# Kernel tuning notes

Hardware: AMD Instinct MI355X
Metric: run time of the kernel (lower is better)

Reference implementation:

```python
import jax, jax.numpy as jnp
import numpy as np
from jax import lax

B, L, D, H = 32, 32, 512, 512
NEG = jnp.float32(-1e9)


def setup_inputs() -> dict:
    key = jax.random.key(0)
    k1, k2, k3, k4, k5 = jax.random.split(key, 5)
    return {
        "inp": jax.random.normal(k1, (B, L, D), jnp.float32),
        "length": jax.random.randint(k2, (B,), 2, L + 1),
        "W_word": jax.random.normal(k3, (D, 2 * H), jnp.float32) * np.float32(np.sqrt(2.0 / D)),
        "b_word": jnp.zeros((2 * H,), jnp.float32),
        "W_comp": jax.random.normal(k4, (2 * H, 5 * H), jnp.float32) * np.float32(np.sqrt(2.0 / (2 * H))),
        "b_comp": jnp.zeros((5 * H,), jnp.float32),
        "comp_query": jax.random.normal(k5, (H,), jnp.float32) * np.float32(0.01),
    }


def _forward(inp, length, W_word, b_word, W_comp, b_comp, comp_query):
    # length_mask[b, t] = 1 if t < length[b]
    length_mask = (jnp.arange(L)[None, :] < length[:, None]).astype(jnp.float32)  # (B, L)
    # leaf states from word_linear: (B, L, 2H) -> h, c
    hc = inp @ W_word + b_word
    h0, c0 = jnp.split(hc, 2, axis=-1)  # each (B, L, H)

    def cell(hl, cl, hr, cr):
        # BinaryTreeLSTMLayer: cat -> 5H gates
        g = jnp.concatenate([hl, hr], axis=-1) @ W_comp + b_comp  # (B, L-1, 5H)
        ig, fl, fr, u, o = jnp.split(g, 5, axis=-1)
        c = cl * jax.nn.sigmoid(fl + 1.0) + cr * jax.nn.sigmoid(fr + 1.0) + jnp.tanh(u) * jax.nn.sigmoid(ig)
        h = jax.nn.sigmoid(o) * jnp.tanh(c)
        return h, c

    def step(carry, i):
        # Fixed-shape (B, L, H) carry; valid length shrinks by 1 each step,
        # tail is zero-padded garbage never selected thanks to masks.
        h, c = carry
        hl, hr = h[:, :-1, :], h[:, 1:, :]
        cl, cr = c[:, :-1, :], c[:, 1:, :]
        nh, nc = cell(hl, cl, hr, cr)  # (B, L-1, H) candidate parents
        # greedy (eval-mode) top-1 composition selection
        logits = jnp.einsum('blh,h->bl', nh, comp_query)
        cand = (jnp.arange(L - 1)[None, :] < (length[:, None] - 1 - i)).astype(jnp.float32)
        sel = jax.nn.one_hot(jnp.argmax(jnp.where(cand > 0, logits, NEG), axis=1), L - 1, dtype=jnp.float32)
        cum = jnp.cumsum(sel, axis=1)
        left = 1.0 - cum
        right = jnp.concatenate([jnp.zeros((B, 1), jnp.float32), cum[:, :-1]], axis=1)
        ch = sel[..., None] * nh + left[..., None] * hl + right[..., None] * hr
        cc = sel[..., None] * nc + left[..., None] * cl + right[..., None] * cr
        sel_h = jnp.sum(sel[..., None] * ch, axis=1)  # (B, H) selected composed node
        is_last = (i == L - 2)  # final merge skips selection (single candidate)
        uh = jnp.where(is_last, nh, ch)
        uc = jnp.where(is_last, nc, cc)
        done = length_mask[:, i + 1][:, None, None]  # 1 if this sample still merging
        nhst = done * uh + (1.0 - done) * h[:, :-1, :]
        ncst = done * uc + (1.0 - done) * c[:, :-1, :]
        pad = jnp.zeros((B, 1, H), jnp.float32)
        h2 = jnp.concatenate([nhst, pad], axis=1)
        c2 = jnp.concatenate([ncst, pad], axis=1)
        node = jnp.where(is_last, h2[:, 0, :], sel_h)
        return (h2, c2), node

    (hf, cf), nodes_rest = lax.scan(step, (h0, c0), jnp.arange(L - 1))
    nodes = jnp.concatenate([h0, jnp.swapaxes(nodes_rest, 0, 1)], axis=1)  # (B, 2L-1, H)
    return hf[:, 0, :], cf[:, 0, :], nodes


def reference(inp, length, W_word, b_word, W_comp, b_comp, comp_query):
    return _forward(inp, length, W_word, b_word, W_comp, b_comp, comp_query)
```

## Files before the change

kernel.cpp:

```cpp
#include <hip/hip_runtime.h>
#include <math.h>

constexpr int NB = 32, NL = 32, ND = 512, NHID = 512, NSTEPS = 31;
constexpr int NC5 = 2560;
constexpr int BH = NB * NHID;
constexpr int HSLOT_Z = 32;
constexpr int NBLK = 160;
constexpr int NGEMM = 80;

constexpr float INV2048 = 1.f / 2048.f;

typedef _Float16 half8  __attribute__((ext_vector_type(8)));
typedef _Float16 half4  __attribute__((ext_vector_type(4)));
typedef float    f32x16 __attribute__((ext_vector_type(16)));
typedef unsigned long long u64;

constexpr size_t OFF_GRAW = 0;
constexpr size_t OFF_PNH  = OFF_GRAW + (size_t)32 * 32 * 2560;
constexpr size_t OFF_PNC  = OFF_PNH + (size_t)31 * 32 * 512;
constexpr size_t OFF_CST  = OFF_PNC + (size_t)31 * 32 * 512;
constexpr size_t OFF_HHI  = OFF_CST + (size_t)33 * 32 * 512;
constexpr size_t OFF_HLO  = OFF_HHI + (size_t)64 * 32 * 512 / 2;
constexpr size_t OFF_WTH  = OFF_HLO + (size_t)64 * 32 * 512 / 2;
constexpr size_t OFF_WTL  = OFF_WTH + (size_t)NC5 * 1024 / 2;
constexpr size_t OFF_INT  = OFF_WTL + (size_t)NC5 * 1024 / 2;
constexpr size_t OFF_LIST = OFF_INT + 8192;

__device__ __forceinline__ float sigf(float x) { return 1.f / (1.f + expf(-x)); }

__device__ __forceinline__ int ld_sc(const int* p) {
    return __hip_atomic_load(p, __ATOMIC_RELAXED, __HIP_MEMORY_SCOPE_AGENT);
}
__device__ __forceinline__ u64 ld_sc64(const void* p) {
    return __hip_atomic_load((const u64*)p, __ATOMIC_RELAXED, __HIP_MEMORY_SCOPE_AGENT);
}
__device__ __forceinline__ void st_sc64(void* p, u64 v) {
    __hip_atomic_store((u64*)p, v, __ATOMIC_RELAXED, __HIP_MEMORY_SCOPE_AGENT);
}
__device__ __forceinline__ u64 packf2(float a, float b) {
    return (u64)__float_as_uint(a) | ((u64)__float_as_uint(b) << 32);
}
__device__ __forceinline__ float2 uf2(u64 v) {
    float2 r;
    r.x = __uint_as_float((unsigned)v);
    r.y = __uint_as_float((unsigned)(v >> 32));
    return r;
}

__device__ __forceinline__ unsigned pack_e(int b, int slot, int l, int r) {
    return (unsigned)b | ((unsigned)slot << 5) | ((unsigned)l << 10) | ((unsigned)r << 16);
}

__global__ __launch_bounds__(256) void init_kernel(
    int* __restrict__ ireg, u64* __restrict__ elist,
    _Float16* __restrict__ hHi, _Float16* __restrict__ hLo, float* __restrict__ cSt)
{
    const int blk = blockIdx.x, tid = threadIdx.x;
    if (blk < 32) {
        if (tid < 31) {
            unsigned e = (unsigned)blk | ((unsigned)tid << 5) |
                         ((unsigned)tid << 10) | ((unsigned)(tid + 1) << 16);
            elist[tid * 32 + blk] = (u64)e;
        }
    } else if (blk == 32) {
        const size_t zb = (size_t)HSLOT_Z * NB * NHID;
        for (int i = tid; i < NB * NHID; i += 256) {
            hHi[zb + i] = (_Float16)0.f;
            hLo[zb + i] = (_Float16)0.f;
            cSt[zb + i] = 0.f;
        }
    } else {
        for (int i = tid; i < 8192; i += 256) ireg[i] = 0;
    }
}

__global__ __launch_bounds__(256) void wsplit_kernel(
    const float* __restrict__ W, _Float16* __restrict__ Wth, _Float16* __restrict__ Wtl)
{
    __shared__ float t[32][33];
    const int n0 = blockIdx.x * 32, k0 = blockIdx.y * 32;
    const int tid = threadIdx.x;
    const int c = tid & 31, r8 = tid >> 5;
#pragma unroll
    for (int p = 0; p < 4; ++p) {
        int r = p * 8 + r8;
        t[r][c] = W[(size_t)(k0 + r) * NC5 + n0 + c];
    }
    __syncthreads();
    const int nl = tid >> 3, k4 = (tid & 7) * 4;
    half4 vh, vl;
#pragma unroll
    for (int i = 0; i < 4; ++i) {
        float v = t[k4 + i][nl];
        _Float16 hh = (_Float16)v;
        vh[i] = hh;
        vl[i] = (_Float16)((v - (float)hh) * 2048.f);
    }
    size_t o = (size_t)(n0 + nl) * 1024 + k0 + k4;
    *(half4*)&Wth[o] = vh;
    *(half4*)&Wtl[o] = vl;
}

__global__ __launch_bounds__(256) void word_gemm64(
    const float* __restrict__ A, const float* __restrict__ W,
    const float* __restrict__ bias,
    _Float16* __restrict__ hi0, _Float16* __restrict__ lo0,
    float* __restrict__ cst, float* __restrict__ out)
{
    const int m0 = blockIdx.x * 64;
    const int n0 = blockIdx.y * 64;
    const int tid = threadIdx.x;
    const int tx = tid & 15, ty = tid >> 4;
    __shared__ float As[16][64];
    __shared__ float Bs[16][64];
    float acc[4][4];
#pragma unroll
    for (int i = 0; i < 4; ++i)
#pragma unroll
        for (int j = 0; j < 4; ++j) acc[i][j] = 0.f;

    for (int kt = 0; kt < ND; kt += 16) {
        {
            int row = tid >> 2, kq = tid & 3;
            float4 v = *(const float4*)(A + (size_t)(m0 + row) * ND + kt + kq * 4);
            As[kq * 4 + 0][row] = v.x;
            As[kq * 4 + 1][row] = v.y;
            As[kq * 4 + 2][row] = v.z;
            As[kq * 4 + 3][row] = v.w;
            int kr = tid >> 4, nq = tid & 15;
            float4 vb = *(const float4*)(W + (size_t)(kt + kr) * 1024 + n0 + nq * 4);
            *(float4*)&Bs[kr][nq * 4] = vb;
        }
        __syncthreads();
#pragma unroll
        for (int kk = 0; kk < 16; ++kk) {
            float a0 = As[kk][ty * 4 + 0], a1 = As[kk][ty * 4 + 1];
            float a2 = As[kk][ty * 4 + 2], a3 = As[kk][ty * 4 + 3];
            float4 bv = *(float4*)&Bs[kk][tx * 4];
            acc[0][0] = fmaf(a0, bv.x, acc[0][0]); acc[0][1] = fmaf(a0, bv.y, acc[0][1]);
            acc[0][2] = fmaf(a0, bv.z, acc[0][2]); acc[0][3] = fmaf(a0, bv.w, acc[0][3]);
            acc[1][0] = fmaf(a1, bv.x, acc[1][0]); acc[1][1] = fmaf(a1, bv.y, acc[1][1]);
            acc[1][2] = fmaf(a1, bv.z, acc[1][2]); acc[1][3] = fmaf(a1, bv.w, acc[1][3]);
            acc[2][0] = fmaf(a2, bv.x, acc[2][0]); acc[2][1] = fmaf(a2, bv.y, acc[2][1]);
            acc[2][2] = fmaf(a2, bv.z, acc[2][2]); acc[2][3] = fmaf(a2, bv.w, acc[2][3]);
            acc[3][0] = fmaf(a3, bv.x, acc[3][0]); acc[3][1] = fmaf(a3, bv.y, acc[3][1]);
            acc[3][2] = fmaf(a3, bv.z, acc[3][2]); acc[3][3] = fmaf(a3, bv.w, acc[3][3]);
        }
        __syncthreads();
    }
    float* nodes = out + 2 * BH;
#pragma unroll
    for (int i = 0; i < 4; ++i) {
        int r = m0 + ty * 4 + i;
        int b = r >> 5, l = r & 31;
#pragma unroll
        for (int jn = 0; jn < 4; ++jn) {
            int n = n0 + tx * 4 + jn;
            float v = acc[i][jn] + bias[n];
            if (n < NHID) {
                size_t si = ((size_t)l * NB + b) * NHID + n;
                _Float16 hh = (_Float16)v;
                hi0[si] = hh;
                lo0[si] = (_Float16)((v - (float)hh) * 2048.f);
                nodes[((size_t)b * 63 + l) * NHID + n] = v;
            } else {
                cst[((size_t)l * NB + b) * NHID + (n - NHID)] = v;
            }
        }
    }
}

__global__ __launch_bounds__(256, 1) void tree_loop(
    _Float16* __restrict__ hHi, _Float16* __restrict__ hLo,
    const _Float16* __restrict__ Wth, const _Float16* __restrict__ Wtl,
    float* __restrict__ graw, const float* __restrict__ bias,
    const float* __restrict__ q, const int* __restrict__ len,
    float* __restrict__ pnh, float* __restrict__ pnc, float* __restrict__ cSt,
    u64* __restrict__ elist, int* __restrict__ ireg, float* __restrict__ out)
{
    const int nt = blockIdx.x;
    const int tid = threadIdx.x;
    const int col = nt % NGEMM;
    const int kw = tid >> 6;
    const int lane = tid & 63;
    const int l5 = lane >> 5, ln = lane & 31;

    int* gd = ireg;

    __shared__ float red[4][32][32];
    __shared__ unsigned s_entry[64];
    __shared__ int s_pidx[32], s_hidx[32], s_cidx[32];
    __shared__ float s_plog[32];
    __shared__ int s_k;
    __shared__ int s_prevk;

    const _Float16* bHiP = Wth + (size_t)(col * 32 + ln) * 1024 + (kw << 8) + l5 * 8;
    const _Float16* bLoP = Wtl + (size_t)(col * 32 + ln) * 1024 + (kw << 8) + l5 * 8;
    half8 Bh[16], Bl[16];
#pragma unroll
    for (int ks = 0; ks < 16; ++ks) {
        Bh[ks] = *(const half8*)(bHiP + ks * 16);
        Bl[ks] = *(const half8*)(bLoP + ks * 16);
    }

    auto gemm_tile = [&](const unsigned* se) {
        {
            const unsigned e = se[ln];
            const int db = e & 31;
            const int lsl = (e >> 10) & 63, rsl = (e >> 16) & 63;
            const int hs = (kw < 2) ? lsl : rsl;
            const int koff = ((kw & 1) << 8) + l5 * 8;
            const _Float16* aHiP = hHi + ((size_t)hs * NB + db) * NHID + koff;
            const _Float16* aLoP = hLo + ((size_t)hs * NB + db) * NHID + koff;
            f32x16 acc1 = (f32x16)0.f, acc2 = (f32x16)0.f;
#pragma unroll
            for (int ks = 0; ks < 16; ++ks) {
                half8 Ah = *(const half8*)(aHiP + ks * 16);
                half8 Al = *(const half8*)(aLoP + ks * 16);
                acc1 = __builtin_amdgcn_mfma_f32_32x32x16_f16(Ah, Bh[ks], acc1, 0, 0, 0);
                acc2 = __builtin_amdgcn_mfma_f32_32x32x16_f16(Ah, Bl[ks], acc2, 0, 0, 0);
                acc2 = __builtin_amdgcn_mfma_f32_32x32x16_f16(Al, Bh[ks], acc2, 0, 0, 0);
            }
#pragma unroll
            for (int a = 0; a < 16; ++a) {
                int row = (a & 3) + 8 * (a >> 2) + 4 * l5;
                red[kw][row][ln] = acc1[a] + acc2[a] * INV2048;
            }
        }
        __syncthreads();
        {
            const int row = tid >> 3, c0 = (tid & 7) * 4;
            const unsigned er = se[row];
            const int rb = er & 31, rslot = (er >> 5) & 31;
            float4 s;
            s.x = (red[0][row][c0+0] + red[1][row][c0+0]) + (red[2][row][c0+0] + red[3][row][c0+0]);
            s.y = (red[0][row][c0+1] + red[1][row][c0+1]) + (red[2][row][c0+1] + red[3][row][c0+1]);
            s.z = (red[0][row][c0+2] + red[1][row][c0+2]) + (red[2][row][c0+2] + red[3][row][c0+2]);
            s.w = (red[0][row][c0+3] + red[1][row][c0+3]) + (red[2][row][c0+3] + red[3][row][c0+3]);
            float* gp = &graw[((size_t)rslot * NB + rb) * NC5 + col * 32 + c0];
            st_sc64(gp,     packf2(s.x, s.y));
            st_sc64(gp + 2, packf2(s.z, s.w));
        }
        __syncthreads();
    };

    __syncthreads();
    {
        const int par = nt / NGEMM;
        for (int mt = par; mt < 31; mt += 2) {
            if (tid < 32) s_entry[tid] = (unsigned)ld_sc64(&elist[mt * 32 + tid]);
            __syncthreads();
            gemm_tile(s_entry);
        }
        if (tid == 0) {
            asm volatile("s_waitcnt vmcnt(0)" ::: "memory");
            __hip_atomic_fetch_add(&gd[(nt & 3) * 32], 1, __ATOMIC_RELAXED,
                                   __HIP_MEMORY_SCOPE_AGENT);
        }
    }
    if (nt >= 112) return;

    if (nt < NGEMM) {
        for (int step = 1; step < NSTEPS; ++step) {
            if (tid < 64) {
                u64 e;
                while ((int)((e = ld_sc64(&elist[tid])) >> 32) < step)
                    __builtin_amdgcn_s_sleep(1);
                s_entry[tid] = (unsigned)e;
            }
            __syncthreads();
            gemm_tile(s_entry);
            gemm_tile(s_entry + 32);
            if (tid == 0) {
                asm volatile("s_waitcnt vmcnt(0)" ::: "memory");
                __hip_atomic_fetch_add(&gd[(nt & 3) * 32], 1, __ATOMIC_RELAXED,
                                       __HIP_MEMORY_SCOPE_AGENT);
            }
        }
        return;
    }

    {
        const int b = nt - NGEMM;
        const int lenb = len[b];
        if (tid < 32) { s_pidx[tid] = min(tid, 30); s_hidx[tid] = tid; s_cidx[tid] = tid; }
        if (tid == 0) s_prevk = -1;
        __syncthreads();

        for (int step = 0; step < NSTEPS; ++step) {
            if (tid < 4) {
                const int tgt = 40 + 20 * step;
                while (ld_sc(&gd[tid * 32]) < tgt) __builtin_amdgcn_s_sleep(1);
            }
            __syncthreads();

            const int pk = s_prevk;
            int nf;
            if (step == 0) nf = 31; else if (pk < 0) nf = 0; else nf = (pk >= 1) ? 2 : 1;
            for (int f = kw; f < nf; f += 4) {
                const int j = (step == 0) ? f : (pk - (nf - 1) + f);
                const int slot = s_pidx[j];
                const int lc = s_cidx[j], rc2 = s_cidx[j + 1];
                const float* gr  = graw + ((size_t)slot * NB + b) * NC5;
                const float* clp = cSt + ((size_t)lc * NB + b) * NHID;
                const float* crp = cSt + ((size_t)rc2 * NB + b) * NHID;
                float lpart = 0.f;
#pragma unroll
                for (int i = 0; i < 4; ++i) {
                    const int h = 2 * lane + 128 * i;
                    float2 g0 = uf2(ld_sc64(gr + h));
                    float2 g1 = uf2(ld_sc64(gr + 512 + h));
                    float2 g2 = uf2(ld_sc64(gr + 1024 + h));
                    float2 g3 = uf2(ld_sc64(gr + 1536 + h));
                    float2 g4 = uf2(ld_sc64(gr + 2048 + h));
                    const float2 b0 = *(const float2*)(bias + h);
                    const float2 b1 = *(const float2*)(bias + 512 + h);
                    const float2 b2 = *(const float2*)(bias + 1024 + h);
                    const float2 b3 = *(const float2*)(bias + 1536 + h);
                    const float2 b4 = *(const float2*)(bias + 2048 + h);
                    const float2 cl2 = *(const float2*)(clp + h);
                    const float2 cr2 = *(const float2*)(crp + h);
                    const float2 q2  = *(const float2*)(q + h);
                    float2 hv, cv;
                    {
                        float c = cl2.x * sigf(g1.x + b1.x + 1.f) + cr2.x * sigf(g2.x + b2.x + 1.f)
                                + tanhf(g3.x + b3.x) * sigf(g0.x + b0.x);
                        float hh = sigf(g4.x + b4.x) * tanhf(c);
                        cv.x = c; hv.x = hh;
                    }
                    {
                        float c = cl2.y * sigf(g1.y + b1.y + 1.f) + cr2.y * sigf(g2.y + b2.y + 1.f)
                                + tanhf(g3.y + b3.y) * sigf(g0.y + b0.y);
                        float hh = sigf(g4.y + b4.y) * tanhf(c);
                        cv.y = c; hv.y = hh;
                    }
                    const size_t po = ((size_t)slot * NB + b) * NHID + h;
                    *(float2*)(pnh + po) = hv;
                    *(float2*)(pnc + po) = cv;
                    lpart = fmaf(hv.x, q2.x, lpart);
                    lpart = fmaf(hv.y, q2.y, lpart);
                }
#pragma unroll
                for (int off = 32; off > 0; off >>= 1) lpart += __shfl_down(lpart, off);
                if (lane == 0) s_plog[slot] = lpart;
            }
            __syncthreads();

            const int actb = lenb - 1 - step;
            const int merge = actb >= 1;
            if (tid < 64) {
                float v = -1e30f;
                int idx = tid;
                if (tid < actb && tid < 31) v = s_plog[s_pidx[tid]];
#pragma unroll
                for (int off = 32; off > 0; off >>= 1) {
                    float ov = __shfl_down(v, off);
                    int   oi = __shfl_down(idx, off);
                    if (ov > v || (ov == v && oi < idx)) { v = ov; idx = oi; }
                }
                if (tid == 0) s_k = idx;
            }
            __syncthreads();
            const int k = s_k;
            const int last = (step == NSTEPS - 1);
            const int NSLOT = 33 + step;

            float* noderow = out + 2 * BH + ((size_t)b * 63 + 32 + step) * NHID;
            if (merge) {
                const int kslot = s_pidx[k];
                const int csl = s_cidx[k];
                if (tid < 128) {
                    const int h0 = tid * 4;
                    const size_t pb = ((size_t)kslot * NB + b) * NHID + h0;
                    float4 x4 = *(const float4*)&pnh[pb];
                    float4 c4 = *(const float4*)&pnc[pb];
                    half4 hv, lv;
#pragma unroll
                    for (int i = 0; i < 4; ++i) {
                        float x = (&x4.x)[i];
                        _Float16 hh = (_Float16)x;
                        hv[i] = hh;
                        lv[i] = (_Float16)((x - (float)hh) * 2048.f);
                    }
                    const size_t so = ((size_t)NSLOT * NB + b) * NHID + h0;
                    st_sc64(&hHi[so], __builtin_bit_cast(u64, hv));
                    st_sc64(&hLo[so], __builtin_bit_cast(u64, lv));
                    *(float4*)&cSt[((size_t)csl * NB + b) * NHID + h0] = c4;
                    *(float4*)&noderow[h0] = x4;
                    if (last) {
                        *(float4*)&out[b * NHID + h0] = x4;
                        *(float4*)&out[BH + b * NHID + h0] = c4;
                    }
                }
            } else {
                const int s0p = s_pidx[0], s0h = s_hidx[0], s0c = s_cidx[0];
                if (tid < 128) {
                    const int h0 = tid * 4;
                    if (!last) {
                        *(float4*)&noderow[h0] =
                            *(const float4*)&pnh[((size_t)s0p * NB + b) * NHID + h0];
                    } else {
                        const size_t so = ((size_t)s0h * NB + b) * NHID + h0;
                        half4 hv = __builtin_bit_cast(half4, ld_sc64(&hHi[so]));
                        half4 lv = __builtin_bit_cast(half4, ld_sc64(&hLo[so]));
                        float4 x4;
#pragma unroll
                        for (int i = 0; i < 4; ++i)
                            (&x4.x)[i] = (float)hv[i] + (float)lv[i] * INV2048;
                        *(float4*)&noderow[h0] = x4;
                        *(float4*)&out[b * NHID + h0] = x4;
                        *(float4*)&out[BH + b * NHID + h0] =
                            *(const float4*)&cSt[((size_t)s0c * NB + b) * NHID + h0];
                    }
                }
            }
            __syncthreads();

            if (tid == 0) {
                const unsigned dummy = pack_e(b, 31, HSLOT_Z, HSLOT_Z);
                if (merge) {
                    unsigned e1 = pack_e(b, s_pidx[k], NSLOT,
                                         (k + 2 <= 31) ? s_hidx[k + 2] : HSLOT_Z);
                    unsigned e0 = (k >= 1)
                        ? pack_e(b, s_pidx[k - 1], s_hidx[k - 1], NSLOT) : dummy;
                    if (!last) {
                        const u64 st = (u64)(step + 1) << 32;
                        st_sc64(&elist[2 * b],     (u64)e0 | st);
                        st_sc64(&elist[2 * b + 1], (u64)e1 | st);
                    }
                    const int recycP = s_pidx[k + 1];
                    for (int j2 = k + 1; j2 <= 29; ++j2) s_pidx[j2] = s_pidx[j2 + 1];
                    if (k < 30) s_pidx[30] = recycP;
                    s_hidx[k] = NSLOT;
                    for (int pp = k + 1; pp <= 30; ++pp) s_hidx[pp] = s_hidx[pp + 1];
                    s_hidx[31] = HSLOT_Z;
                    for (int pp = k + 1; pp <= 30; ++pp) s_cidx[pp] = s_cidx[pp + 1];
                    s_cidx[31] = HSLOT_Z;
                    s_prevk = k;
                } else {
                    if (!last) {
                        const u64 st = (u64)(step + 1) << 32;
                        st_sc64(&elist[2 * b],     (u64)dummy | st);
                        st_sc64(&elist[2 * b + 1], (u64)dummy | st);
                    }
                    s_prevk = -1;
                }
            }
        }
    }
}

extern "C" void kernel_launch(void* const* d_in, const int* in_sizes, int n_in,
                              void* d_out, int out_size, void* d_ws, size_t ws_size,
                              hipStream_t stream) {
    const float* inp    = (const float*)d_in[0];
    const int*   length = (const int*)d_in[1];
    const float* W_word = (const float*)d_in[2];
    const float* b_word = (const float*)d_in[3];
    const float* W_comp = (const float*)d_in[4];
    const float* b_comp = (const float*)d_in[5];
    const float* q      = (const float*)d_in[6];
    float* out = (float*)d_out;
    float* ws  = (float*)d_ws;

    float*     graw = ws + OFF_GRAW;
    float*     pnh  = ws + OFF_PNH;
    float*     pnc  = ws + OFF_PNC;
    float*     cSt  = ws + OFF_CST;
    _Float16*  hHi  = (_Float16*)(ws + OFF_HHI);
    _Float16*  hLo  = (_Float16*)(ws + OFF_HLO);
    _Float16*  Wth  = (_Float16*)(ws + OFF_WTH);
    _Float16*  Wtl  = (_Float16*)(ws + OFF_WTL);
    int*       ireg = (int*)(ws + OFF_INT);
    u64*       elist = (u64*)(ws + OFF_LIST);

    init_kernel<<<34, 256, 0, stream>>>(ireg, elist, hHi, hLo, cSt);
    wsplit_kernel<<<dim3(NC5 / 32, 1024 / 32), 256, 0, stream>>>(W_comp, Wth, Wtl);
    word_gemm64<<<dim3(16, 16), 256, 0, stream>>>(inp, W_word, b_word,
                                                  hHi, hLo, cSt, out);
    tree_loop<<<NBLK, 256, 0, stream>>>(hHi, hLo, Wth, Wtl, graw, b_comp, q, length,
                                        pnh, pnc, cSt, elist, ireg, out);
}
```

Before: 766.0 us.

## Fuse LSTM cell epilogue into per-block GEMM tiles with unit-permuted weights

Weights are permuted so each of 128 blocks owns 4 hidden units across all 5 gates. This lets every block compute the LSTM cell, the cell state and a partial selection logit directly after its MFMA tile, instead of writing raw gates to global memory for separate controller blocks to read. Cell state stays block-local and fresh candidate slots replace the recycled ones, so the final nodes, h and c are assembled by a new gather kernel from a selection log. The cost is more workspace, an extra permutation kernel and a gather pass, and each controller must now reduce 128 logit partials across blocks.

```diff
diff --git a/kernel.cpp b/kernel.cpp
--- a/kernel.cpp
+++ b/kernel.cpp
@@ -1,12 +1,13 @@
 #include <hip/hip_runtime.h>
 #include <math.h>
 
-constexpr int NB = 32, NL = 32, ND = 512, NHID = 512, NSTEPS = 31;
+constexpr int NB = 32, ND = 512, NHID = 512, NSTEPS = 31;
 constexpr int NC5 = 2560;
 constexpr int BH = NB * NHID;
-constexpr int HSLOT_Z = 32;
-constexpr int NBLK = 160;
-constexpr int NGEMM = 80;
+constexpr int SLOT_Z = 32;
+constexpr int SLOT_DUMMY = 126;
+constexpr int NSLOTS = 128;
+constexpr int NBLK = 128;
 
 constexpr float INV2048 = 1.f / 2048.f;
 
@@ -15,16 +16,22 @@
 typedef float    f32x16 __attribute__((ext_vector_type(16)));
 typedef unsigned long long u64;
 
-constexpr size_t OFF_GRAW = 0;
-constexpr size_t OFF_PNH  = OFF_GRAW + (size_t)32 * 32 * 2560;
-constexpr size_t OFF_PNC  = OFF_PNH + (size_t)31 * 32 * 512;
-constexpr size_t OFF_CST  = OFF_PNC + (size_t)31 * 32 * 512;
-constexpr size_t OFF_HHI  = OFF_CST + (size_t)33 * 32 * 512;
-constexpr size_t OFF_HLO  = OFF_HHI + (size_t)64 * 32 * 512 / 2;
-constexpr size_t OFF_WTH  = OFF_HLO + (size_t)64 * 32 * 512 / 2;
+constexpr size_t OFF_WTH  = 0;
 constexpr size_t OFF_WTL  = OFF_WTH + (size_t)NC5 * 1024 / 2;
-constexpr size_t OFF_INT  = OFF_WTL + (size_t)NC5 * 1024 / 2;
-constexpr size_t OFF_LIST = OFF_INT + 8192;
+constexpr size_t OFF_WPH  = OFF_WTL + (size_t)NC5 * 1024 / 2;
+constexpr size_t OFF_WPL  = OFF_WPH + (size_t)128 * 32 * 1024 / 2;
+constexpr size_t OFF_HHI  = OFF_WPL + (size_t)128 * 32 * 1024 / 2;
+constexpr size_t OFF_HLO  = OFF_HHI + (size_t)NSLOTS * 32 * 512 / 2;
+constexpr size_t OFF_HF32 = OFF_HLO + (size_t)NSLOTS * 32 * 512 / 2;
+constexpr size_t OFF_CST  = OFF_HF32 + (size_t)NSLOTS * 32 * 512;
+constexpr size_t OFF_CLOC = OFF_CST + (size_t)32 * 32 * 512;
+constexpr size_t OFF_LPART= OFF_CLOC + (size_t)128 * NSLOTS * 32 * 4;
+constexpr size_t OFF_SEL  = OFF_LPART + (size_t)NSLOTS * 32 * 128;
+constexpr size_t OFF_ELIST= OFF_SEL + 1024;
+constexpr size_t OFF_IREG = OFF_ELIST + 4096;
+
+constexpr int IR_GD = 0;
+constexpr int IR_E0 = 256;
 
 __device__ __forceinline__ float sigf(float x) { return 1.f / (1.f + expf(-x)); }
 
@@ -37,40 +44,35 @@
 __device__ __forceinline__ void st_sc64(void* p, u64 v) {
     __hip_atomic_store((u64*)p, v, __ATOMIC_RELAXED, __HIP_MEMORY_SCOPE_AGENT);
 }
-__device__ __forceinline__ u64 packf2(float a, float b) {
-    return (u64)__float_as_uint(a) | ((u64)__float_as_uint(b) << 32);
-}
-__device__ __forceinline__ float2 uf2(u64 v) {
-    float2 r;
-    r.x = __uint_as_float((unsigned)v);
-    r.y = __uint_as_float((unsigned)(v >> 32));
-    return r;
-}
-
-__device__ __forceinline__ unsigned pack_e(int b, int slot, int l, int r) {
-    return (unsigned)b | ((unsigned)slot << 5) | ((unsigned)l << 10) | ((unsigned)r << 16);
+__device__ __forceinline__ void st_sc32f(void* p, float v) {
+    __hip_atomic_store((int*)p, __float_as_int(v), __ATOMIC_RELAXED, __HIP_MEMORY_SCOPE_AGENT);
+}
+__device__ __forceinline__ void st_sc32i(void* p, int v) {
+    __hip_atomic_store((int*)p, v, __ATOMIC_RELAXED, __HIP_MEMORY_SCOPE_AGENT);
+}
+__device__ __forceinline__ unsigned pack_e(int b, int cand, int l, int r) {
+    return (unsigned)b | ((unsigned)cand << 5) | ((unsigned)l << 12) | ((unsigned)r << 19);
 }
 
 __global__ __launch_bounds__(256) void init_kernel(
     int* __restrict__ ireg, u64* __restrict__ elist,
-    _Float16* __restrict__ hHi, _Float16* __restrict__ hLo, float* __restrict__ cSt)
+    _Float16* __restrict__ hHi, _Float16* __restrict__ hLo)
 {
     const int blk = blockIdx.x, tid = threadIdx.x;
-    if (blk < 32) {
-        if (tid < 31) {
-            unsigned e = (unsigned)blk | ((unsigned)tid << 5) |
-                         ((unsigned)tid << 10) | ((unsigned)(tid + 1) << 16);
-            elist[tid * 32 + blk] = (u64)e;
-        }
-    } else if (blk == 32) {
-        const size_t zb = (size_t)HSLOT_Z * NB * NHID;
-        for (int i = tid; i < NB * NHID; i += 256) {
+    if (blk == 0) {
+        for (int i = tid; i < 128; i += 256) ireg[IR_GD + i] = 0;
+        for (int i = tid; i < 992; i += 256) {
+            int t = i >> 5, b = i & 31;
+            ireg[IR_E0 + i] = (int)pack_e(b, 33 + t, t, t + 1);
+        }
+    } else if (blk == 1) {
+        for (int i = tid; i < 31 * 64; i += 256) elist[i] = 0ull;
+    } else {
+        const size_t zb = ((size_t)SLOT_Z * 32) * 512;
+        for (int i = tid + (blk - 2) * 256; i < 32 * 512; i += 512) {
             hHi[zb + i] = (_Float16)0.f;
             hLo[zb + i] = (_Float16)0.f;
-            cSt[zb + i] = 0.f;
-        }
-    } else {
-        for (int i = tid; i < 8192; i += 256) ireg[i] = 0;
+        }
     }
 }
 
@@ -99,6 +101,27 @@
     size_t o = (size_t)(n0 + nl) * 1024 + k0 + k4;
     *(half4*)&Wth[o] = vh;
     *(half4*)&Wtl[o] = vl;
+}
+
+__global__ __launch_bounds__(256) void wperm_kernel(
+    const _Float16* __restrict__ Wth, const _Float16* __restrict__ Wtl,
+    _Float16* __restrict__ WpH, _Float16* __restrict__ WpL)
+{
+    const int blk = blockIdx.x;
+    const int tid = threadIdx.x;
+    const int k4 = tid * 4;
+    for (int c = 0; c < 32; ++c) {
+        half4 vh = (half4)(_Float16)0.f, vl = (half4)(_Float16)0.f;
+        if (c < 20) {
+            int unit = blk * 4 + c / 5, g = c % 5;
+            size_t src = (size_t)(g * 512 + unit) * 1024 + k4;
+            vh = *(const half4*)&Wth[src];
+            vl = *(const half4*)&Wtl[src];
+        }
+        size_t dst = ((size_t)blk * 32 + c) * 1024 + k4;
+        *(half4*)&WpH[dst] = vh;
+        *(half4*)&WpL[dst] = vl;
+    }
 }
 
 __global__ __launch_bounds__(256) void word_gemm64(
@@ -171,31 +194,33 @@
 }
 
 __global__ __launch_bounds__(256, 1) void tree_loop(
-    _Float16* __restrict__ hHi, _Float16* __restrict__ hLo,
-    const _Float16* __restrict__ Wth, const _Float16* __restrict__ Wtl,
-    float* __restrict__ graw, const float* __restrict__ bias,
-    const float* __restrict__ q, const int* __restrict__ len,
-    float* __restrict__ pnh, float* __restrict__ pnc, float* __restrict__ cSt,
-    u64* __restrict__ elist, int* __restrict__ ireg, float* __restrict__ out)
+    _Float16* __restrict__ hHi, _Float16* __restrict__ hLo, float* __restrict__ hF32,
+    const _Float16* __restrict__ WpH, const _Float16* __restrict__ WpL,
+    const float* __restrict__ bias, const float* __restrict__ q,
+    const int* __restrict__ len, const float* __restrict__ cst,
+    float* __restrict__ cLoc, float* __restrict__ lpart,
+    u64* __restrict__ elist, int* __restrict__ selLog, int* __restrict__ ireg)
 {
-    const int nt = blockIdx.x;
+    const int blk = blockIdx.x;
     const int tid = threadIdx.x;
-    const int col = nt % NGEMM;
-    const int kw = tid >> 6;
-    const int lane = tid & 63;
+    const int kw = tid >> 6, lane = tid & 63;
     const int l5 = lane >> 5, ln = lane & 31;
 
-    int* gd = ireg;
+    int* gd = ireg + IR_GD;
+    const int* E0 = ireg + IR_E0;
 
     __shared__ float red[4][32][32];
     __shared__ unsigned s_entry[64];
-    __shared__ int s_pidx[32], s_hidx[32], s_cidx[32];
-    __shared__ float s_plog[32];
-    __shared__ int s_k;
-    __shared__ int s_prevk;
-
-    const _Float16* bHiP = Wth + (size_t)(col * 32 + ln) * 1024 + (kw << 8) + l5 * 8;
-    const _Float16* bLoP = Wtl + (size_t)(col * 32 + ln) * 1024 + (kw << 8) + l5 * 8;
+    __shared__ float sH[32][4];
+    __shared__ float sLP[32];
+    __shared__ float sBias[4][5];
+    __shared__ float sQ[4];
+    __shared__ float s_plog[128];
+    __shared__ int s_pidx[32], s_hidx[32];
+    __shared__ int s_k, s_prevk;
+
+    const _Float16* bHiP = WpH + ((size_t)blk * 32 + ln) * 1024 + (kw << 8) + l5 * 8;
+    const _Float16* bLoP = WpL + ((size_t)blk * 32 + ln) * 1024 + (kw << 8) + l5 * 8;
     half8 Bh[16], Bl[16];
 #pragma unroll
     for (int ks = 0; ks < 16; ++ks) {
@@ -203,146 +228,162 @@
         Bl[ks] = *(const half8*)(bLoP + ks * 16);
     }
 
-    auto gemm_tile = [&](const unsigned* se) {
-        {
-            const unsigned e = se[ln];
-            const int db = e & 31;
-            const int lsl = (e >> 10) & 63, rsl = (e >> 16) & 63;
-            const int hs = (kw < 2) ? lsl : rsl;
-            const int koff = ((kw & 1) << 8) + l5 * 8;
-            const _Float16* aHiP = hHi + ((size_t)hs * NB + db) * NHID + koff;
-            const _Float16* aLoP = hLo + ((size_t)hs * NB + db) * NHID + koff;
-            f32x16 acc1 = (f32x16)0.f, acc2 = (f32x16)0.f;
-#pragma unroll
-            for (int ks = 0; ks < 16; ++ks) {
-                half8 Ah = *(const half8*)(aHiP + ks * 16);
-                half8 Al = *(const half8*)(aLoP + ks * 16);
-                acc1 = __builtin_amdgcn_mfma_f32_32x32x16_f16(Ah, Bh[ks], acc1, 0, 0, 0);
-                acc2 = __builtin_amdgcn_mfma_f32_32x32x16_f16(Ah, Bl[ks], acc2, 0, 0, 0);
-                acc2 = __builtin_amdgcn_mfma_f32_32x32x16_f16(Al, Bh[ks], acc2, 0, 0, 0);
-            }
-#pragma unroll
-            for (int a = 0; a < 16; ++a) {
-                int row = (a & 3) + 8 * (a >> 2) + 4 * l5;
-                red[kw][row][ln] = acc1[a] + acc2[a] * INV2048;
-            }
-        }
-        __syncthreads();
-        {
-            const int row = tid >> 3, c0 = (tid & 7) * 4;
-            const unsigned er = se[row];
-            const int rb = er & 31, rslot = (er >> 5) & 31;
-            float4 s;
-            s.x = (red[0][row][c0+0] + red[1][row][c0+0]) + (red[2][row][c0+0] + red[3][row][c0+0]);
-            s.y = (red[0][row][c0+1] + red[1][row][c0+1]) + (red[2][row][c0+1] + red[3][row][c0+1]);
-            s.z = (red[0][row][c0+2] + red[1][row][c0+2]) + (red[2][row][c0+2] + red[3][row][c0+2]);
-            s.w = (red[0][row][c0+3] + red[1][row][c0+3]) + (red[2][row][c0+3] + red[3][row][c0+3]);
-            float* gp = &graw[((size_t)rslot * NB + rb) * NC5 + col * 32 + c0];
-            st_sc64(gp,     packf2(s.x, s.y));
-            st_sc64(gp + 2, packf2(s.z, s.w));
-        }
-        __syncthreads();
-    };
-
+    if (tid < 20) { int ul = tid / 5, g = tid % 5; sBias[ul][g] = bias[g * 512 + blk * 4 + ul]; }
+    if (tid >= 32 && tid < 36) sQ[tid - 32] = q[blk * 4 + (tid - 32)];
+
+    float* cB = cLoc + (size_t)blk * NSLOTS * 32 * 4;
+    for (int i = tid; i < 33 * 32 * 4; i += 256) {
+        int slot = i >> 7, rem = i & 127;
+        int b = rem >> 2, ul = rem & 3;
+        cB[i] = (slot == SLOT_Z) ? 0.f
+                                 : cst[((size_t)slot * 32 + b) * 512 + blk * 4 + ul];
+    }
+
+    int lenb = 0;
+    if (blk < NB) {
+        if (tid < 31) s_pidx[tid] = 33 + tid;
+        if (tid < 32) s_hidx[tid] = tid;
+        if (tid == 0) s_prevk = 0;
+        lenb = len[blk];
+    }
     __syncthreads();
-    {
-        const int par = nt / NGEMM;
-        for (int mt = par; mt < 31; mt += 2) {
-            if (tid < 32) s_entry[tid] = (unsigned)ld_sc64(&elist[mt * 32 + tid]);
-            __syncthreads();
-            gemm_tile(s_entry);
+
+    for (int step = 0; step < NSTEPS; ++step) {
+        int ntiles;
+        if (step == 0) {
+            ntiles = 31;
+        } else {
+            ntiles = 2;
+            if (tid < 64) {
+                u64 e;
+                while ((int)((e = ld_sc64(&elist[step * 64 + tid])) >> 32) < step)
+                    __builtin_amdgcn_s_sleep(4);
+                s_entry[tid] = (unsigned)e;
+            }
+            __syncthreads();
+        }
+
+        for (int t = 0; t < ntiles; ++t) {
+            if (step == 0) {
+                if (tid < 32) s_entry[tid] = (unsigned)E0[t * 32 + tid];
+                __syncthreads();
+            }
+            const unsigned* se = (step == 0) ? s_entry : s_entry + t * 32;
+            {
+                const unsigned e = se[ln];
+                const int eb = e & 31;
+                const int lsl = (e >> 12) & 127, rsl = (e >> 19) & 127;
+                const int hs = (kw < 2) ? lsl : rsl;
+                const int koff = ((kw & 1) << 8) + l5 * 8;
+                const _Float16* aHiP = hHi + ((size_t)hs * 32 + eb) * 512 + koff;
+                const _Float16* aLoP = hLo + ((size_t)hs * 32 + eb) * 512 + koff;
+                f32x16 acc1 = (f32x16)0.f, acc2 = (f32x16)0.f;
+#pragma unroll
+                for (int ks = 0; ks < 16; ++ks) {
+                    half8 Ah = *(const half8*)(aHiP + ks * 16);
+                    half8 Al = *(const half8*)(aLoP + ks * 16);
+                    acc1 = __builtin_amdgcn_mfma_f32_32x32x16_f16(Ah, Bh[ks], acc1, 0, 0, 0);
+                    acc2 = __builtin_amdgcn_mfma_f32_32x32x16_f16(Ah, Bl[ks], acc2, 0, 0, 0);
+                    acc2 = __builtin_amdgcn_mfma_f32_32x32x16_f16(Al, Bh[ks], acc2, 0, 0, 0);
+                }
+#pragma unroll
+                for (int a = 0; a < 16; ++a) {
+                    int row = (a & 3) + 8 * (a >> 2) + 4 * l5;
+                    red[kw][row][ln] = acc1[a] + acc2[a] * INV2048;
+                }
+            }
+            __syncthreads();
+            if (tid < 128) {
+                const int r = tid >> 2, ul = tid & 3;
+                const unsigned e = se[r];
+                const int eb = e & 31, cand = (e >> 5) & 127;
+                const int lsl = (e >> 12) & 127, rsl = (e >> 19) & 127;
+                const int c0 = ul * 5;
+                float g0 = (red[0][r][c0+0] + red[1][r][c0+0]) + (red[2][r][c0+0] + red[3][r][c0+0]);
+                float g1 = (red[0][r][c0+1] + red[1][r][c0+1]) + (red[2][r][c0+1] + red[3][r][c0+1]);
+                float g2 = (red[0][r][c0+2] + red[1][r][c0+2]) + (red[2][r][c0+2] + red[3][r][c0+2]);
+                float g3 = (red[0][r][c0+3] + red[1][r][c0+3]) + (red[2][r][c0+3] + red[3][r][c0+3]);
+                float g4 = (red[0][r][c0+4] + red[1][r][c0+4]) + (red[2][r][c0+4] + red[3][r][c0+4]);
+                float ig = g0 + sBias[ul][0];
+                float fl = g1 + sBias[ul][1];
+                float fr = g2 + sBias[ul][2];
+                float uu = g3 + sBias[ul][3];
+                float oo = g4 + sBias[ul][4];
+                float cl = cB[lsl * 128 + eb * 4 + ul];
+                float cr = cB[rsl * 128 + eb * 4 + ul];
+                float c = cl * sigf(fl + 1.f) + cr * sigf(fr + 1.f) + tanhf(uu) * sigf(ig);
+                float h = sigf(oo) * tanhf(c);
+                cB[cand * 128 + eb * 4 + ul] = c;
+                sH[r][ul] = h;
+                float p = h * sQ[ul];
+                p += __shfl_down(p, 1);
+                p += __shfl_down(p, 2);
+                if (ul == 0) sLP[r] = p;
+            }
+            __syncthreads();
+            if (tid < 32) {
+                const unsigned e = se[tid];
+                const int eb = e & 31, cand = (e >> 5) & 127;
+                float x0 = sH[tid][0], x1 = sH[tid][1], x2 = sH[tid][2], x3 = sH[tid][3];
+                half4 hv, lv;
+                {
+                    _Float16 h0 = (_Float16)x0, h1 = (_Float16)x1,
+                             h2 = (_Float16)x2, h3 = (_Float16)x3;
+                    hv[0] = h0; hv[1] = h1; hv[2] = h2; hv[3] = h3;
+                    lv[0] = (_Float16)((x0 - (float)h0) * 2048.f);
+                    lv[1] = (_Float16)((x1 - (float)h1) * 2048.f);
+                    lv[2] = (_Float16)((x2 - (float)h2) * 2048.f);
+                    lv[3] = (_Float16)((x3 - (float)h3) * 2048.f);
+                }
+                const size_t so = ((size_t)cand * 32 + eb) * 512 + blk * 4;
+                st_sc64(&hHi[so], __builtin_bit_cast(u64, hv));
+                st_sc64(&hLo[so], __builtin_bit_cast(u64, lv));
+                u64 f01 = (u64)__float_as_uint(x0) | ((u64)__float_as_uint(x1) << 32);
+                u64 f23 = (u64)__float_as_uint(x2) | ((u64)__float_as_uint(x3) << 32);
+                st_sc64(&hF32[so], f01);
+                st_sc64(&hF32[so + 2], f23);
+                st_sc32f(&lpart[((size_t)cand * 32 + eb) * 128 + blk], sLP[tid]);
+            }
+            __syncthreads();
         }
         if (tid == 0) {
             asm volatile("s_waitcnt vmcnt(0)" ::: "memory");
-            __hip_atomic_fetch_add(&gd[(nt & 3) * 32], 1, __ATOMIC_RELAXED,
+            __hip_atomic_fetch_add(&gd[(blk & 3) * 32], 1, __ATOMIC_RELAXED,
                                    __HIP_MEMORY_SCOPE_AGENT);
         }
-    }
-    if (nt >= 112) return;
-
-    if (nt < NGEMM) {
-        for (int step = 1; step < NSTEPS; ++step) {
-            if (tid < 64) {
-                u64 e;
-                while ((int)((e = ld_sc64(&elist[tid])) >> 32) < step)
-                    __builtin_amdgcn_s_sleep(1);
-                s_entry[tid] = (unsigned)e;
-            }
-            __syncthreads();
-            gemm_tile(s_entry);
-            gemm_tile(s_entry + 32);
-            if (tid == 0) {
-                asm volatile("s_waitcnt vmcnt(0)" ::: "memory");
-                __hip_atomic_fetch_add(&gd[(nt & 3) * 32], 1, __ATOMIC_RELAXED,
-                                       __HIP_MEMORY_SCOPE_AGENT);
-            }
-        }
-        return;
-    }
-
-    {
-        const int b = nt - NGEMM;
-        const int lenb = len[b];
-        if (tid < 32) { s_pidx[tid] = min(tid, 30); s_hidx[tid] = tid; s_cidx[tid] = tid; }
-        if (tid == 0) s_prevk = -1;
-        __syncthreads();
-
-        for (int step = 0; step < NSTEPS; ++step) {
+
+        if (blk < NB) {
+            const int b = blk;
             if (tid < 4) {
-                const int tgt = 40 + 20 * step;
-                while (ld_sc(&gd[tid * 32]) < tgt) __builtin_amdgcn_s_sleep(1);
-            }
-            __syncthreads();
-
-            const int pk = s_prevk;
-            int nf;
-            if (step == 0) nf = 31; else if (pk < 0) nf = 0; else nf = (pk >= 1) ? 2 : 1;
-            for (int f = kw; f < nf; f += 4) {
-                const int j = (step == 0) ? f : (pk - (nf - 1) + f);
-                const int slot = s_pidx[j];
-                const int lc = s_cidx[j], rc2 = s_cidx[j + 1];
-                const float* gr  = graw + ((size_t)slot * NB + b) * NC5;
-                const float* clp = cSt + ((size_t)lc * NB + b) * NHID;
-                const float* crp = cSt + ((size_t)rc2 * NB + b) * NHID;
-                float lpart = 0.f;
-#pragma unroll
-                for (int i = 0; i < 4; ++i) {
-                    const int h = 2 * lane + 128 * i;
-                    float2 g0 = uf2(ld_sc64(gr + h));
-                    float2 g1 = uf2(ld_sc64(gr + 512 + h));
-                    float2 g2 = uf2(ld_sc64(gr + 1024 + h));
-                    float2 g3 = uf2(ld_sc64(gr + 1536 + h));
-                    float2 g4 = uf2(ld_sc64(gr + 2048 + h));
-                    const float2 b0 = *(const float2*)(bias + h);
-                    const float2 b1 = *(const float2*)(bias + 512 + h);
-                    const float2 b2 = *(const float2*)(bias + 1024 + h);
-                    const float2 b3 = *(const float2*)(bias + 1536 + h);
-                    const float2 b4 = *(const float2*)(bias + 2048 + h);
-                    const float2 cl2 = *(const float2*)(clp + h);
-                    const float2 cr2 = *(const float2*)(crp + h);
-                    const float2 q2  = *(const float2*)(q + h);
-                    float2 hv, cv;
-                    {
-                        float c = cl2.x * sigf(g1.x + b1.x + 1.f) + cr2.x * sigf(g2.x + b2.x + 1.f)
-                                + tanhf(g3.x + b3.x) * sigf(g0.x + b0.x);
-                        float hh = sigf(g4.x + b4.x) * tanhf(c);
-                        cv.x = c; hv.x = hh;
+                const int tgt = 32 * (step + 1);
+                while (ld_sc(&gd[tid * 32]) < tgt) __builtin_amdgcn_s_sleep(2);
+            }
+            __syncthreads();
+            if (step == 0) {
+                if (tid < 64) {
+                    for (int j = 0; j < 31; ++j) {
+                        const int cand = 33 + j;
+                        const float* pp = lpart + ((size_t)cand * 32 + b) * 128;
+                        float v = pp[tid] + pp[tid + 64];
+#pragma unroll
+                        for (int off = 32; off > 0; off >>= 1) v += __shfl_down(v, off);
+                        if (tid == 0) s_plog[cand] = v;
                     }
-                    {
-                        float c = cl2.y * sigf(g1.y + b1.y + 1.f) + cr2.y * sigf(g2.y + b2.y + 1.f)
-                                + tanhf(g3.y + b3.y) * sigf(g0.y + b0.y);
-                        float hh = sigf(g4.y + b4.y) * tanhf(c);
-                        cv.y = c; hv.y = hh;
+                }
+            } else {
+                const int pk = s_prevk;
+                const int nf = (pk < 0) ? 0 : ((pk >= 1) ? 2 : 1);
+                if (tid < 64) {
+                    for (int f = 0; f < nf; ++f) {
+                        const int pos = pk - (nf - 1) + f;
+                        const int cand = s_pidx[pos];
+                        const float* pp = lpart + ((size_t)cand * 32 + b) * 128;
+                        float v = pp[tid] + pp[tid + 64];
+#pragma unroll
+                        for (int off = 32; off > 0; off >>= 1) v += __shfl_down(v, off);
+                        if (tid == 0) s_plog[cand] = v;
                     }
-                    const size_t po = ((size_t)slot * NB + b) * NHID + h;
-                    *(float2*)(pnh + po) = hv;
-                    *(float2*)(pnc + po) = cv;
-                    lpart = fmaf(hv.x, q2.x, lpart);
-                    lpart = fmaf(hv.y, q2.y, lpart);
-                }
-#pragma unroll
-                for (int off = 32; off > 0; off >>= 1) lpart += __shfl_down(lpart, off);
-                if (lane == 0) s_plog[slot] = lpart;
+                }
             }
             __syncthreads();
 
@@ -363,90 +404,72 @@
             __syncthreads();
             const int k = s_k;
             const int last = (step == NSTEPS - 1);
-            const int NSLOT = 33 + step;
-
-            float* noderow = out + 2 * BH + ((size_t)b * 63 + 32 + step) * NHID;
-            if (merge) {
-                const int kslot = s_pidx[k];
-                const int csl = s_cidx[k];
-                if (tid < 128) {
-                    const int h0 = tid * 4;
-                    const size_t pb = ((size_t)kslot * NB + b) * NHID + h0;
-                    float4 x4 = *(const float4*)&pnh[pb];
-                    float4 c4 = *(const float4*)&pnc[pb];
-                    half4 hv, lv;
-#pragma unroll
-                    for (int i = 0; i < 4; ++i) {
-                        float x = (&x4.x)[i];
-                        _Float16 hh = (_Float16)x;
-                        hv[i] = hh;
-                        lv[i] = (_Float16)((x - (float)hh) * 2048.f);
-                    }
-                    const size_t so = ((size_t)NSLOT * NB + b) * NHID + h0;
-                    st_sc64(&hHi[so], __builtin_bit_cast(u64, hv));
-                    st_sc64(&hLo[so], __builtin_bit_cast(u64, lv));
-                    *(float4*)&cSt[((size_t)csl * NB + b) * NHID + h0] = c4;
-                    *(float4*)&noderow[h0] = x4;
-                    if (last) {
-                        *(float4*)&out[b * NHID + h0] = x4;
-                        *(float4*)&out[BH + b * NHID + h0] = c4;
-                    }
-                }
-            } else {
-                const int s0p = s_pidx[0], s0h = s_hidx[0], s0c = s_cidx[0];
-                if (tid < 128) {
-                    const int h0 = tid * 4;
-                    if (!last) {
-                        *(float4*)&noderow[h0] =
-                            *(const float4*)&pnh[((size_t)s0p * NB + b) * NHID + h0];
-                    } else {
-                        const size_t so = ((size_t)s0h * NB + b) * NHID + h0;
-                        half4 hv = __builtin_bit_cast(half4, ld_sc64(&hHi[so]));
-                        half4 lv = __builtin_bit_cast(half4, ld_sc64(&hLo[so]));
-                        float4 x4;
-#pragma unroll
-                        for (int i = 0; i < 4; ++i)
-                            (&x4.x)[i] = (float)hv[i] + (float)lv[i] * INV2048;
-                        *(float4*)&noderow[h0] = x4;
-                        *(float4*)&out[b * NHID + h0] = x4;
-                        *(float4*)&out[BH + b * NHID + h0] =
-                            *(const float4*)&cSt[((size_t)s0c * NB + b) * NHID + h0];
-                    }
-                }
-            }
-            __syncthreads();
 
             if (tid == 0) {
-                const unsigned dummy = pack_e(b, 31, HSLOT_Z, HSLOT_Z);
                 if (merge) {
-                    unsigned e1 = pack_e(b, s_pidx[k], NSLOT,
-                                         (k + 2 <= 31) ? s_hidx[k + 2] : HSLOT_Z);
-                    unsigned e0 = (k >= 1)
-                        ? pack_e(b, s_pidx[k - 1], s_hidx[k - 1], NSLOT) : dummy;
+                    const int winner = s_pidx[k];
+                    const int candA = 64 + 2 * step, candB = 65 + 2 * step;
                     if (!last) {
                         const u64 st = (u64)(step + 1) << 32;
-                        st_sc64(&elist[2 * b],     (u64)e0 | st);
-                        st_sc64(&elist[2 * b + 1], (u64)e1 | st);
+                        unsigned e0 = (k >= 1)
+                            ? pack_e(b, candA, s_hidx[k - 1], winner)
+                            : pack_e(b, SLOT_DUMMY, SLOT_Z, SLOT_Z);
+                        unsigned e1 = pack_e(b, candB, winner,
+                                             (k + 2 <= 31) ? s_hidx[k + 2] : SLOT_Z);
+                        st_sc64(&elist[(step + 1) * 64 + 2 * b],     (u64)e0 | st);
+                        st_sc64(&elist[(step + 1) * 64 + 2 * b + 1], (u64)e1 | st);
                     }
-                    const int recycP = s_pidx[k + 1];
-                    for (int j2 = k + 1; j2 <= 29; ++j2) s_pidx[j2] = s_pidx[j2 + 1];
-                    if (k < 30) s_pidx[30] = recycP;
-                    s_hidx[k] = NSLOT;
-                    for (int pp = k + 1; pp <= 30; ++pp) s_hidx[pp] = s_hidx[pp + 1];
-                    s_hidx[31] = HSLOT_Z;
-                    for (int pp = k + 1; pp <= 30; ++pp) s_cidx[pp] = s_cidx[pp + 1];
-                    s_cidx[31] = HSLOT_Z;
+                    st_sc32i(&selLog[step * 32 + b], winner);
+                    if (k >= 1) s_pidx[k - 1] = candA;
+                    s_pidx[k] = candB;
+                    s_hidx[k] = winner;
+                    for (int j = k + 1; j <= 30; ++j) s_hidx[j] = s_hidx[j + 1];
+                    s_hidx[31] = SLOT_Z;
+                    for (int j = k + 1; j <= 29; ++j) s_pidx[j] = s_pidx[j + 1];
                     s_prevk = k;
                 } else {
                     if (!last) {
                         const u64 st = (u64)(step + 1) << 32;
-                        st_sc64(&elist[2 * b],     (u64)dummy | st);
-                        st_sc64(&elist[2 * b + 1], (u64)dummy | st);
+                        const unsigned d = pack_e(b, SLOT_DUMMY, SLOT_Z, SLOT_Z);
+                        st_sc64(&elist[(step + 1) * 64 + 2 * b],     (u64)d | st);
+                        st_sc64(&elist[(step + 1) * 64 + 2 * b + 1], (u64)d | st);
                     }
+                    st_sc32i(&selLog[step * 32 + b], last ? s_hidx[0] : s_pidx[0]);
                     s_prevk = -1;
                 }
             }
-        }
+            __syncthreads();
+        }
+    }
+}
+
+__global__ __launch_bounds__(256) void gather_kernel(
+    const float* __restrict__ hF32, const float* __restrict__ cst,
+    const float* __restrict__ cLoc, const int* __restrict__ selLog,
+    float* __restrict__ out)
+{
+    const int b = blockIdx.x;
+    const int tid = threadIdx.x;
+    float* nodes = out + 2 * BH;
+    for (int s = 0; s < NSTEPS; ++s) {
+        const int id = selLog[s * 32 + b];
+        float* dst = nodes + ((size_t)b * 63 + 32 + s) * 512;
+        const float* src = (id < 32) ? nodes + ((size_t)b * 63 + id) * 512
+                                     : hF32 + ((size_t)id * 32 + b) * 512;
+        for (int u = tid; u < 512; u += 256) dst[u] = src[u];
+    }
+    const int rid = selLog[30 * 32 + b];
+    const float* hsrc = (rid < 32) ? nodes + ((size_t)b * 63 + rid) * 512
+                                   : hF32 + ((size_t)rid * 32 + b) * 512;
+    for (int u = tid; u < 512; u += 256) {
+        out[b * 512 + u] = hsrc[u];
+        float cv;
+        if (rid < 32) {
+            cv = cst[((size_t)rid * 32 + b) * 512 + u];
+        } else {
+            cv = cLoc[(size_t)(u >> 2) * NSLOTS * 32 * 4 + (size_t)rid * 128 + b * 4 + (u & 3)];
+        }
+        out[BH + b * 512 + u] = cv;
     }
 }
 
@@ -463,21 +486,26 @@
     float* out = (float*)d_out;
     float* ws  = (float*)d_ws;
 
-    float*     graw = ws + OFF_GRAW;
-    float*     pnh  = ws + OFF_PNH;
-    float*     pnc  = ws + OFF_PNC;
-    float*     cSt  = ws + OFF_CST;
+    _Float16*  Wth  = (_Float16*)(ws + OFF_WTH);
+    _Float16*  Wtl  = (_Float16*)(ws + OFF_WTL);
+    _Float16*  WpH  = (_Float16*)(ws + OFF_WPH);
+    _Float16*  WpL  = (_Float16*)(ws + OFF_WPL);
     _Float16*  hHi  = (_Float16*)(ws + OFF_HHI);
     _Float16*  hLo  = (_Float16*)(ws + OFF_HLO);
-    _Float16*  Wth  = (_Float16*)(ws + OFF_WTH);
-    _Float16*  Wtl  = (_Float16*)(ws + OFF_WTL);
-    int*       ireg = (int*)(ws + OFF_INT);
-    u64*       elist = (u64*)(ws + OFF_LIST);
-
-    init_kernel<<<34, 256, 0, stream>>>(ireg, elist, hHi, hLo, cSt);
+    float*     hF32 = ws + OFF_HF32;
+    float*     cst  = ws + OFF_CST;
+    float*     cLoc = ws + OFF_CLOC;
+    float*     lpart= ws + OFF_LPART;
+    int*       selLog = (int*)(ws + OFF_SEL);
+    u64*       elist  = (u64*)(ws + OFF_ELIST);
+    int*       ireg   = (int*)(ws + OFF_IREG);
+
+    init_kernel<<<4, 256, 0, stream>>>(ireg, elist, hHi, hLo);
     wsplit_kernel<<<dim3(NC5 / 32, 1024 / 32), 256, 0, stream>>>(W_comp, Wth, Wtl);
+    wperm_kernel<<<128, 256, 0, stream>>>(Wth, Wtl, WpH, WpL);
     word_gemm64<<<dim3(16, 16), 256, 0, stream>>>(inp, W_word, b_word,
-                                                  hHi, hLo, cSt, out);
-    tree_loop<<<NBLK, 256, 0, stream>>>(hHi, hLo, Wth, Wtl, graw, b_comp, q, length,
-                                        pnh, pnc, cSt, elist, ireg, out);
-}
+                                                  hHi, hLo, cst, out);
+    tree_loop<<<NBLK, 256, 0, stream>>>(hHi, hLo, hF32, WpH, WpL, b_comp, q, length,
+                                        cst, cLoc, lpart, elist, selLog, ireg);
+    gather_kernel<<<NB, 256, 0, stream>>>(hF32, cst, cLoc, selLog, out);
+}
```

After: 783.5 us. 1.02x slower.
